# Kernel tuning notes

Hardware: AMD Instinct MI355X
Metric: run time of the kernel (lower is better)

Reference implementation:

```python
import jax, jax.numpy as jnp
import numpy as np

B, L, E, D1, D2 = 256, 128, 64, 512, 512


def setup_inputs() -> dict:
    key = jax.random.key(0)
    k1, k2, k3, kw = jax.random.split(key, 4)
    tensor1 = jax.random.normal(k1, (B, L, D1), dtype=jnp.float32)
    tensor2 = jax.random.normal(k2, (B, L, D2), dtype=jnp.float32)
    parameters_index = jax.random.randint(k3, (B,), 0, E, dtype=jnp.int32)
    # xavier_uniform with relu gain: gain*sqrt(6/(fan_in+fan_out)),
    # torch fan for [E,D1,D2]: fan_in = D1*D2, fan_out = E*D2
    gain = float(np.sqrt(2.0))
    bound = gain * float(np.sqrt(6.0 / (D1 * D2 + E * D2)))
    weights = jax.random.uniform(kw, (E, D1, D2), minval=-bound, maxval=bound, dtype=jnp.float32)
    return {"tensor1": tensor1, "tensor2": tensor2, "parameters_index": parameters_index, "weights": weights}


def reference(tensor1, tensor2, parameters_index, weights):
    # gather per-batch weight matrix [B, D1, D2], then bilinear form x1^T W x2
    w = weights[parameters_index]  # [B, D1, D2]
    # equals: sum over i,j of tensor1[b,l,i] * w[b,i,j] * tensor2[b,l,j] -> [B, L]
    return jnp.einsum('bli,bij,blj->bl', tensor1, w, tensor2)
```

## Files before the change

kernel.cpp:

```cpp
#include <hip/hip_runtime.h>
#include <stdint.h>

#define NB 256
#define NL 128
#define ND1 512
#define ND2 512

#define BI 64
#define NKT 16

typedef float float4_t __attribute__((ext_vector_type(4)));
typedef __bf16 bf16x8_t __attribute__((ext_vector_type(8)));
typedef unsigned short ushort8_t __attribute__((ext_vector_type(8)));

__device__ __forceinline__ unsigned short f2bf(float f) {
    unsigned int u = __float_as_uint(f);
    u += 0x7FFFu + ((u >> 16) & 1u);
    return (unsigned short)(u >> 16);
}

__global__ __launch_bounds__(512, 4) void pdot_kernel(
    const float* __restrict__ t1, const float* __restrict__ t2,
    const int* __restrict__ pidx, const float* __restrict__ wgt,
    float* __restrict__ out)
{
    __shared__ unsigned short sW[BI * ND2];

    const int g  = blockIdx.x;
    const int b  = g & (NB - 1);
    const int it = g >> 8;
    const int i0 = it * BI;

    const int t  = threadIdx.x;
    const int wv = t >> 6;
    const int ln = t & 63;
    const int nh = ln & 15;
    const int qd = ln >> 4;

    const int e = pidx[b];
    const float* wp = wgt + (size_t)e * (ND1 * ND2) + (size_t)i0 * ND2;

    {
        const int r  = t >> 3;
        const int c8 = t & 7;
        const int sw = r & 7;
        const float* src = wp + (size_t)r * ND2;
        unsigned short* dst = &sW[r * ND2];
        #pragma unroll
        for (int q = 0; q < 8; ++q) {
            const int c = c8 + 8 * q;
            float4_t lo = *(const float4_t*)(src + c * 8);
            float4_t hi = *(const float4_t*)(src + c * 8 + 4);
            ushort8_t u;
            u[0] = f2bf(lo.x); u[1] = f2bf(lo.y); u[2] = f2bf(lo.z); u[3] = f2bf(lo.w);
            u[4] = f2bf(hi.x); u[5] = f2bf(hi.y); u[6] = f2bf(hi.z); u[7] = f2bf(hi.w);
            *(ushort8_t*)(dst + ((c ^ sw) * 8)) = u;
        }
    }
    __syncthreads();

    const float* aRow = t2 + (size_t)b * (NL * ND2) + (size_t)(wv * 16 + nh) * ND2;
    const int swz = nh & 7;
    const unsigned short* wBase = &sW[nh * ND2];

    float4_t acc[4];
    #pragma unroll
    for (int ns = 0; ns < 4; ++ns) { float4_t z = {0.f,0.f,0.f,0.f}; acc[ns] = z; }

    float4_t a_lo = *(const float4_t*)(aRow + qd * 8);
    float4_t a_hi = *(const float4_t*)(aRow + qd * 8 + 4);

    #pragma unroll
    for (int kt = 0; kt < NKT; ++kt) {
        float4_t n_lo, n_hi;
        if (kt < NKT - 1) {
            n_lo = *(const float4_t*)(aRow + (kt + 1) * 32 + qd * 8);
            n_hi = *(const float4_t*)(aRow + (kt + 1) * 32 + qd * 8 + 4);
        }
        ushort8_t ua;
        ua[0] = f2bf(a_lo.x); ua[1] = f2bf(a_lo.y); ua[2] = f2bf(a_lo.z); ua[3] = f2bf(a_lo.w);
        ua[4] = f2bf(a_hi.x); ua[5] = f2bf(a_hi.y); ua[6] = f2bf(a_hi.z); ua[7] = f2bf(a_hi.w);
        bf16x8_t af = __builtin_bit_cast(bf16x8_t, ua);

        const int co = ((kt * 4 + qd) ^ swz) * 8;
        #pragma unroll
        for (int ns = 0; ns < 4; ++ns) {
            bf16x8_t bfr = __builtin_bit_cast(bf16x8_t,
                *(const ushort8_t*)(wBase + ns * 16 * ND2 + co));
            acc[ns] = __builtin_amdgcn_mfma_f32_16x16x32_bf16(af, bfr, acc[ns], 0, 0, 0);
        }
        a_lo = n_lo; a_hi = n_hi;
    }

    const float* t1p = t1 + (size_t)b * (NL * ND1) + i0;
    #pragma unroll
    for (int r = 0; r < 4; ++r) {
        const int row = wv * 16 + qd * 4 + r;
        float ps = 0.f;
        #pragma unroll
        for (int ns = 0; ns < 4; ++ns)
            ps += acc[ns][r] * t1p[(size_t)row * ND1 + ns * 16 + nh];
        ps += __shfl_xor(ps, 1);
        ps += __shfl_xor(ps, 2);
        ps += __shfl_xor(ps, 4);
        ps += __shfl_xor(ps, 8);
        if (nh == 0) atomicAdd(&out[b * NL + row], ps);
    }
}

extern "C" void kernel_launch(void* const* d_in, const int* in_sizes, int n_in,
                              void* d_out, int out_size, void* d_ws, size_t ws_size,
                              hipStream_t stream)
{
    const float* t1  = (const float*)d_in[0];
    const float* t2  = (const float*)d_in[1];
    const int* pidx  = (const int*)d_in[2];
    const float* wgt = (const float*)d_in[3];
    float* out = (float*)d_out;

    hipMemsetAsync(out, 0, (size_t)out_size * sizeof(float), stream);
    pdot_kernel<<<dim3(NB * (ND1 / BI)), dim3(512), 0, stream>>>(t1, t2, pidx, wgt, out);
}
```

Baseline: 245.9 us.

## Process one batch per block with register-resident t2 fragments and double-buffered weight tiles

```diff
diff --git a/kernel.cpp b/kernel.cpp
--- a/kernel.cpp
+++ b/kernel.cpp
@@ -7,7 +7,8 @@
 #define ND2 512
 
 #define BI 64
-#define NKT 16
+#define NIT (ND1 / BI)
+#define NKT (ND2 / 32)
 
 typedef float float4_t __attribute__((ext_vector_type(4)));
 typedef __bf16 bf16x8_t __attribute__((ext_vector_type(8)));
@@ -19,92 +20,117 @@
     return (unsigned short)(u >> 16);
 }
 
-__global__ __launch_bounds__(512, 4) void pdot_kernel(
+__device__ __forceinline__ ushort8_t pack8(float4_t lo, float4_t hi) {
+    ushort8_t u;
+    u[0] = f2bf(lo.x); u[1] = f2bf(lo.y); u[2] = f2bf(lo.z); u[3] = f2bf(lo.w);
+    u[4] = f2bf(hi.x); u[5] = f2bf(hi.y); u[6] = f2bf(hi.z); u[7] = f2bf(hi.w);
+    return u;
+}
+
+__global__ __launch_bounds__(1024, 4) void pdot_kernel(
     const float* __restrict__ t1, const float* __restrict__ t2,
     const int* __restrict__ pidx, const float* __restrict__ wgt,
     float* __restrict__ out)
 {
-    __shared__ unsigned short sW[BI * ND2];
+    __shared__ unsigned short sW[2][BI * ND2];
 
-    const int g  = blockIdx.x;
-    const int b  = g & (NB - 1);
-    const int it = g >> 8;
-    const int i0 = it * BI;
-
+    const int b  = blockIdx.x;
     const int t  = threadIdx.x;
     const int wv = t >> 6;
+    const int mg = wv >> 1;
+    const int ng = wv & 1;
     const int ln = t & 63;
     const int nh = ln & 15;
     const int qd = ln >> 4;
 
     const int e = pidx[b];
-    const float* wp = wgt + (size_t)e * (ND1 * ND2) + (size_t)i0 * ND2;
+    const float* wp  = wgt + (size_t)e * (ND1 * ND2);
+    const float* t1p = t1  + (size_t)b * (NL * ND1);
+
+    const int sr  = t >> 4;
+    const int sc  = t & 15;
+    const int ssw = sr & 31;
+
+    const int lrow = mg * 16 + nh;
+    const float* aRow = t2 + (size_t)b * (NL * ND2) + (size_t)lrow * ND2 + qd * 8;
+    bf16x8_t afrag[NKT];
+    #pragma unroll
+    for (int kt = 0; kt < NKT; ++kt) {
+        float4_t lo = *(const float4_t*)(aRow + kt * 32);
+        float4_t hi = *(const float4_t*)(aRow + kt * 32 + 4);
+        afrag[kt] = __builtin_bit_cast(bf16x8_t, pack8(lo, hi));
+    }
 
     {
-        const int r  = t >> 3;
-        const int c8 = t & 7;
-        const int sw = r & 7;
-        const float* src = wp + (size_t)r * ND2;
-        unsigned short* dst = &sW[r * ND2];
+        const float* src = wp + (size_t)sr * ND2;
+        unsigned short* dst = &sW[0][sr * ND2];
         #pragma unroll
-        for (int q = 0; q < 8; ++q) {
-            const int c = c8 + 8 * q;
+        for (int q = 0; q < 4; ++q) {
+            const int c = sc + 16 * q;
             float4_t lo = *(const float4_t*)(src + c * 8);
             float4_t hi = *(const float4_t*)(src + c * 8 + 4);
-            ushort8_t u;
-            u[0] = f2bf(lo.x); u[1] = f2bf(lo.y); u[2] = f2bf(lo.z); u[3] = f2bf(lo.w);
-            u[4] = f2bf(hi.x); u[5] = f2bf(hi.y); u[6] = f2bf(hi.z); u[7] = f2bf(hi.w);
-            *(ushort8_t*)(dst + ((c ^ sw) * 8)) = u;
+            *(ushort8_t*)(dst + (c ^ ssw) * 8) = pack8(lo, hi);
         }
     }
     __syncthreads();
 
-    const float* aRow = t2 + (size_t)b * (NL * ND2) + (size_t)(wv * 16 + nh) * ND2;
-    const int swz = nh & 7;
-    const unsigned short* wBase = &sW[nh * ND2];
+    const int r0 = ng * 32 + nh;
+    const int r1 = ng * 32 + 16 + nh;
+    const unsigned short* wb0base;
+    const int sw0 = r0 & 31;
+    const int sw1 = r1 & 31;
 
-    float4_t acc[4];
-    #pragma unroll
-    for (int ns = 0; ns < 4; ++ns) { float4_t z = {0.f,0.f,0.f,0.f}; acc[ns] = z; }
+    float4_t ps = {0.f, 0.f, 0.f, 0.f};
 
-    float4_t a_lo = *(const float4_t*)(aRow + qd * 8);
-    float4_t a_hi = *(const float4_t*)(aRow + qd * 8 + 4);
+    for (int it = 0; it < NIT; ++it) {
+        const int cur = it & 1;
+
+        if (it < NIT - 1) {
+            const float* src = wp + (size_t)((it + 1) * BI + sr) * ND2;
+            unsigned short* dst = &sW[cur ^ 1][sr * ND2];
+            #pragma unroll
+            for (int q = 0; q < 4; ++q) {
+                const int c = sc + 16 * q;
+                float4_t lo = *(const float4_t*)(src + c * 8);
+                float4_t hi = *(const float4_t*)(src + c * 8 + 4);
+                *(ushort8_t*)(dst + (c ^ ssw) * 8) = pack8(lo, hi);
+            }
+        }
+
+        float4_t acc0 = {0.f, 0.f, 0.f, 0.f};
+        float4_t acc1 = {0.f, 0.f, 0.f, 0.f};
+        const unsigned short* sb = &sW[cur][0];
+        #pragma unroll
+        for (int kt = 0; kt < NKT; ++kt) {
+            const int c = kt * 4 + qd;
+            bf16x8_t b0 = __builtin_bit_cast(bf16x8_t,
+                *(const ushort8_t*)(sb + r0 * ND2 + (c ^ sw0) * 8));
+            acc0 = __builtin_amdgcn_mfma_f32_16x16x32_bf16(afrag[kt], b0, acc0, 0, 0, 0);
+            bf16x8_t b1 = __builtin_bit_cast(bf16x8_t,
+                *(const ushort8_t*)(sb + r1 * ND2 + (c ^ sw1) * 8));
+            acc1 = __builtin_amdgcn_mfma_f32_16x16x32_bf16(afrag[kt], b1, acc1, 0, 0, 0);
+        }
+
+        const int colbase = it * BI + ng * 32;
+        #pragma unroll
+        for (int r = 0; r < 4; ++r) {
+            const int row = mg * 16 + qd * 4 + r;
+            ps[r] += acc0[r] * t1p[(size_t)row * ND1 + colbase + nh]
+                   + acc1[r] * t1p[(size_t)row * ND1 + colbase + 16 + nh];
+        }
+
+        __syncthreads();
+    }
+    (void)wb0base;
 
     #pragma unroll
-    for (int kt = 0; kt < NKT; ++kt) {
-        float4_t n_lo, n_hi;
-        if (kt < NKT - 1) {
-            n_lo = *(const float4_t*)(aRow + (kt + 1) * 32 + qd * 8);
-            n_hi = *(const float4_t*)(aRow + (kt + 1) * 32 + qd * 8 + 4);
-        }
-        ushort8_t ua;
-        ua[0] = f2bf(a_lo.x); ua[1] = f2bf(a_lo.y); ua[2] = f2bf(a_lo.z); ua[3] = f2bf(a_lo.w);
-        ua[4] = f2bf(a_hi.x); ua[5] = f2bf(a_hi.y); ua[6] = f2bf(a_hi.z); ua[7] = f2bf(a_hi.w);
-        bf16x8_t af = __builtin_bit_cast(bf16x8_t, ua);
-
-        const int co = ((kt * 4 + qd) ^ swz) * 8;
-        #pragma unroll
-        for (int ns = 0; ns < 4; ++ns) {
-            bf16x8_t bfr = __builtin_bit_cast(bf16x8_t,
-                *(const ushort8_t*)(wBase + ns * 16 * ND2 + co));
-            acc[ns] = __builtin_amdgcn_mfma_f32_16x16x32_bf16(af, bfr, acc[ns], 0, 0, 0);
-        }
-        a_lo = n_lo; a_hi = n_hi;
-    }
-
-    const float* t1p = t1 + (size_t)b * (NL * ND1) + i0;
-    #pragma unroll
     for (int r = 0; r < 4; ++r) {
-        const int row = wv * 16 + qd * 4 + r;
-        float ps = 0.f;
-        #pragma unroll
-        for (int ns = 0; ns < 4; ++ns)
-            ps += acc[ns][r] * t1p[(size_t)row * ND1 + ns * 16 + nh];
-        ps += __shfl_xor(ps, 1);
-        ps += __shfl_xor(ps, 2);
-        ps += __shfl_xor(ps, 4);
-        ps += __shfl_xor(ps, 8);
-        if (nh == 0) atomicAdd(&out[b * NL + row], ps);
+        float v = ps[r];
+        v += __shfl_xor(v, 1);
+        v += __shfl_xor(v, 2);
+        v += __shfl_xor(v, 4);
+        v += __shfl_xor(v, 8);
+        if (nh == 0) atomicAdd(&out[b * NL + mg * 16 + qd * 4 + r], v);
     }
 }
 
@@ -119,5 +145,5 @@
     float* out = (float*)d_out;
 
     hipMemsetAsync(out, 0, (size_t)out_size * sizeof(float), stream);
-    pdot_kernel<<<dim3(NB * (ND1 / BI)), dim3(512), 0, stream>>>(t1, t2, pidx, wgt, out);
+    pdot_kernel<<<dim3(NB), dim3(1024), 0, stream>>>(t1, t2, pidx, wgt, out);
 }
```

Measured after the change: 251.9 us. 2.4% more time.
